# Performance work log

Measured on AMD Instinct MI355X. Metric: run time of the kernel, lower is better.

## Reference

```python
import jax, jax.numpy as jnp
import numpy as np

D, K = 128, 32
B, H, W = 16, 64, 64


def setup_inputs() -> dict:
    key = jax.random.key(0)
    k1, k2, k3 = jax.random.split(key, 3)
    x = jax.random.normal(k1, (B, D, H, W), dtype=jnp.float32)
    std1 = 1.0 / (K * D) ** 0.5
    codewords = jax.random.uniform(k2, (K, D), minval=-std1, maxval=std1, dtype=jnp.float32)
    scale = jax.random.uniform(k3, (K,), minval=-1.0, maxval=0.0, dtype=jnp.float32)
    return {"x": x, "codewords": codewords, "scale": scale}


def reference(x, codewords, scale):
    b = x.shape[0]
    # (B, D, H, W) -> (B, N, D)
    X = x.reshape(b, D, -1).transpose(0, 2, 1)
    # scaled L2: SL[b,n,k] = scale[k] * ||X[b,n] - C[k]||^2, expanded to avoid (B,N,K,D)
    x2 = jnp.sum(X * X, axis=-1)                      # (B, N)
    c2 = jnp.sum(codewords * codewords, axis=-1)      # (K,)
    xc = jnp.einsum('bnd,kd->bnk', X, codewords)      # (B, N, K)
    SL = scale[None, None, :] * (x2[:, :, None] - 2.0 * xc + c2[None, None, :])
    A = jax.nn.softmax(SL, axis=2)                    # (B, N, K)
    # E[b,k,d] = sum_n A[b,n,k] * (X[b,n,d] - C[k,d])
    E = jnp.einsum('bnk,bnd->bkd', A, X) - jnp.sum(A, axis=1)[:, :, None] * codewords[None, :, :]
    return E
```

## Files before the change

### kernel.cpp

```cpp
#include <hip/hip_runtime.h>
#include <hip/hip_bf16.h>


#define D_   128
#define K_   32
#define NPB  64
#define NTOT 4096

typedef __attribute__((ext_vector_type(8))) short bf16x8;
typedef __attribute__((ext_vector_type(4))) float f32x4;

__device__ __forceinline__ short f2b(float f) {
  unsigned u = __float_as_uint(f);
  unsigned r = (u + 0x7FFFu + ((u >> 16) & 1u)) >> 16;
  return (short)r;
}

__global__ __launch_bounds__(256, 4) void enc_kernel(
    const float* __restrict__ x,
    const float* __restrict__ cw,
    const float* __restrict__ scale,
    float* __restrict__ out)
{
  __shared__ __align__(16) float sX[D_ * NPB];
  __shared__ __align__(16) short sAb[K_ * NPB];
  __shared__ float sX2[NPB];
  __shared__ float sasum[K_];

  const int t  = threadIdx.x;
  const int w  = t >> 6;
  const int l  = t & 63;
  const int lr = l & 15;
  const int lg = l >> 4;
  const int b  = blockIdx.x >> 6;
  const int n0 = (blockIdx.x & 63) * NPB;

  if (t < K_) sasum[t] = 0.0f;

  const float* xb = x + (size_t)b * D_ * NTOT + n0;
  float4 xs[8];
  #pragma unroll
  for (int j = 0; j < 8; ++j) {
    int flat = j * 256 + t;
    int d = flat >> 4, n4 = flat & 15;
    xs[j] = *reinterpret_cast<const float4*>(xb + (size_t)d * NTOT + n4 * 4);
  }

  bf16x8 bC[2][4];
  float c2p0 = 0.f, c2p1 = 0.f;
  #pragma unroll
  for (int kt = 0; kt < 2; ++kt) {
    const float* crow = cw + (lr + 16 * kt) * D_ + lg * 8;
    #pragma unroll
    for (int s = 0; s < 4; ++s) {
      float4 v0 = *reinterpret_cast<const float4*>(crow + 32 * s);
      float4 v1 = *reinterpret_cast<const float4*>(crow + 32 * s + 4);
      float vv[8] = {v0.x, v0.y, v0.z, v0.w, v1.x, v1.y, v1.z, v1.w};
      bf16x8 f;
      float cs = 0.f;
      #pragma unroll
      for (int j = 0; j < 8; ++j) { f[j] = f2b(vv[j]); cs = fmaf(vv[j], vv[j], cs); }
      bC[kt][s] = f;
      if (kt == 0) c2p0 += cs; else c2p1 += cs;
    }
  }
  c2p0 += __shfl_xor(c2p0, 16); c2p0 += __shfl_xor(c2p0, 32);
  c2p1 += __shfl_xor(c2p1, 16); c2p1 += __shfl_xor(c2p1, 32);
  const float sc0 = scale[lr];
  const float sc1 = scale[lr + 16];

  float4* sX4 = reinterpret_cast<float4*>(sX);
  #pragma unroll
  for (int j = 0; j < 8; ++j) {
    int flat = j * 256 + t;
    int d = flat >> 4, n4 = flat & 15;
    sX4[d * 16 + (n4 ^ (d & 7))] = xs[j];
  }
  __syncthreads();

  const int m0 = w * 16;
  f32x4 p0 = {0.f, 0.f, 0.f, 0.f}, p1 = {0.f, 0.f, 0.f, 0.f};
  float x2p = 0.f;
  #pragma unroll
  for (int s = 0; s < 4; ++s) {
    int dbase = 32 * s + lg * 8;
    float av[8];
    #pragma unroll
    for (int j = 0; j < 8; ++j) {
      int d = dbase + j;
      av[j] = sX[d * 64 + ((m0 + lr) ^ ((d & 7) << 2))];
    }
    bf16x8 af;
    #pragma unroll
    for (int j = 0; j < 8; ++j) { af[j] = f2b(av[j]); x2p = fmaf(av[j], av[j], x2p); }
    p0 = __builtin_amdgcn_mfma_f32_16x16x32_bf16(af, bC[0][s], p0, 0, 0, 0);
    p1 = __builtin_amdgcn_mfma_f32_16x16x32_bf16(af, bC[1][s], p1, 0, 0, 0);
  }
  x2p += __shfl_xor(x2p, 16);
  x2p += __shfl_xor(x2p, 32);
  if (lg == 0) sX2[m0 + lr] = x2p;
  float x2r[4];
  #pragma unroll
  for (int r = 0; r < 4; ++r) x2r[r] = sX2[m0 + lg * 4 + r];

  float a0[4], a1[4], mr[4], sr[4];
  #pragma unroll
  for (int r = 0; r < 4; ++r) {
    float sl0 = sc0 * (x2r[r] - 2.f * p0[r] + c2p0);
    float sl1 = sc1 * (x2r[r] - 2.f * p1[r] + c2p1);
    a0[r] = sl0; a1[r] = sl1;
    mr[r] = fmaxf(sl0, sl1);
  }
  #pragma unroll
  for (int dlt = 1; dlt <= 8; dlt <<= 1)
    #pragma unroll
    for (int r = 0; r < 4; ++r) mr[r] = fmaxf(mr[r], __shfl_xor(mr[r], dlt));
  #pragma unroll
  for (int r = 0; r < 4; ++r) {
    a0[r] = __expf(a0[r] - mr[r]);
    a1[r] = __expf(a1[r] - mr[r]);
    sr[r] = a0[r] + a1[r];
  }
  #pragma unroll
  for (int dlt = 1; dlt <= 8; dlt <<= 1)
    #pragma unroll
    for (int r = 0; r < 4; ++r) sr[r] += __shfl_xor(sr[r], dlt);
  #pragma unroll
  for (int r = 0; r < 4; ++r) {
    float inv = 1.0f / sr[r];
    a0[r] *= inv; a1[r] *= inv;
  }

  float as0 = a0[0] + a0[1] + a0[2] + a0[3];
  float as1 = a1[0] + a1[1] + a1[2] + a1[3];
  as0 += __shfl_xor(as0, 16); as0 += __shfl_xor(as0, 32);
  as1 += __shfl_xor(as1, 16); as1 += __shfl_xor(as1, 32);
  if (lg == 0) {
    atomicAdd(&sasum[lr], as0);
    atomicAdd(&sasum[lr + 16], as1);
  }
  #pragma unroll
  for (int r = 0; r < 4; ++r) {
    int n = m0 + lg * 4 + r;
    int k0i = lr, k1i = lr + 16;
    sAb[k0i * 64 + (n ^ ((k0i & 7) << 3))] = f2b(a0[r]);
    sAb[k1i * 64 + (n ^ ((k1i & 7) << 3))] = f2b(a1[r]);
  }
  __syncthreads();

  bf16x8 aA[2][2];
  #pragma unroll
  for (int mt = 0; mt < 2; ++mt) {
    int k = mt * 16 + lr;
    #pragma unroll
    for (int s = 0; s < 2; ++s) {
      int nb = 32 * s + lg * 8;
      aA[mt][s] = *reinterpret_cast<const bf16x8*>(
          &sAb[k * 64 + (nb ^ ((k & 7) << 3))]);
    }
  }
  float asv[2][4];
  #pragma unroll
  for (int mt = 0; mt < 2; ++mt)
    #pragma unroll
    for (int r = 0; r < 4; ++r) asv[mt][r] = sasum[mt * 16 + lg * 4 + r];
  f32x4 acc[2][2];
  #pragma unroll
  for (int mt = 0; mt < 2; ++mt)
    #pragma unroll
    for (int dti = 0; dti < 2; ++dti) {
      int d = (2 * w + dti) * 16 + lr;
      #pragma unroll
      for (int r = 0; r < 4; ++r) {
        int k = mt * 16 + lg * 4 + r;
        acc[mt][dti][r] = -asv[mt][r] * cw[k * D_ + d];
      }
    }
  #pragma unroll
  for (int s = 0; s < 2; ++s) {
    #pragma unroll
    for (int dti = 0; dti < 2; ++dti) {
      int d = (2 * w + dti) * 16 + lr;
      int nb = 32 * s + lg * 8;
      int q0 = (nb >> 2) ^ (d & 7);
      int q1 = ((nb >> 2) + 1) ^ (d & 7);
      float4 v0 = sX4[d * 16 + q0];
      float4 v1 = sX4[d * 16 + q1];
      float vv[8] = {v0.x, v0.y, v0.z, v0.w, v1.x, v1.y, v1.z, v1.w};
      bf16x8 bf;
      #pragma unroll
      for (int j = 0; j < 8; ++j) bf[j] = f2b(vv[j]);
      acc[0][dti] = __builtin_amdgcn_mfma_f32_16x16x32_bf16(aA[0][s], bf, acc[0][dti], 0, 0, 0);
      acc[1][dti] = __builtin_amdgcn_mfma_f32_16x16x32_bf16(aA[1][s], bf, acc[1][dti], 0, 0, 0);
    }
  }
  float* op = out + (size_t)b * K_ * D_;
  #pragma unroll
  for (int mt = 0; mt < 2; ++mt)
    #pragma unroll
    for (int dti = 0; dti < 2; ++dti) {
      int d = (2 * w + dti) * 16 + lr;
      #pragma unroll
      for (int r = 0; r < 4; ++r) {
        int k = mt * 16 + lg * 4 + r;
        unsafeAtomicAdd(&op[k * D_ + d], acc[mt][dti][r]);
      }
    }
}

extern "C" void kernel_launch(void* const* d_in, const int* in_sizes, int n_in,
                              void* d_out, int out_size, void* d_ws, size_t ws_size,
                              hipStream_t stream) {
  const float* x  = (const float*)d_in[0];
  const float* cw = (const float*)d_in[1];
  const float* sc = (const float*)d_in[2];
  float* out = (float*)d_out;
  const int B = in_sizes[0] / (D_ * NTOT);
  hipMemsetAsync(d_out, 0, (size_t)out_size * sizeof(float), stream);
  enc_kernel<<<dim3(B * (NTOT / NPB)), dim3(256), 0, stream>>>(x, cw, sc, out);
}
```

Baseline: 92.22 us.

## Store x tile in shared memory as bf16 in both n-major and d-major layouts

```diff
diff --git a/kernel.cpp b/kernel.cpp
--- a/kernel.cpp
+++ b/kernel.cpp
@@ -9,11 +9,10 @@
 
 typedef __attribute__((ext_vector_type(8))) short bf16x8;
 typedef __attribute__((ext_vector_type(4))) float f32x4;
+typedef __attribute__((ext_vector_type(4))) short short4v;
 
 __device__ __forceinline__ short f2b(float f) {
-  unsigned u = __float_as_uint(f);
-  unsigned r = (u + 0x7FFFu + ((u >> 16) & 1u)) >> 16;
-  return (short)r;
+  return (short)__builtin_bit_cast(unsigned short, __float2bfloat16(f));
 }
 
 __global__ __launch_bounds__(256, 4) void enc_kernel(
@@ -22,9 +21,10 @@
     const float* __restrict__ scale,
     float* __restrict__ out)
 {
-  __shared__ __align__(16) float sX[D_ * NPB];
+  __shared__ __align__(16) short sNb[NPB * D_];
+  __shared__ __align__(16) short sDb[D_ * NPB];
   __shared__ __align__(16) short sAb[K_ * NPB];
-  __shared__ float sX2[NPB];
+  __shared__ __align__(16) float sX2w[NPB * 4];
   __shared__ float sasum[K_];
 
   const int t  = threadIdx.x;
@@ -37,13 +37,52 @@
 
   if (t < K_) sasum[t] = 0.0f;
 
+  const int n4s = t & 15;
+  const int d0  = (t >> 4) * 8;
   const float* xb = x + (size_t)b * D_ * NTOT + n0;
   float4 xs[8];
   #pragma unroll
+  for (int j = 0; j < 8; ++j)
+    xs[j] = *reinterpret_cast<const float4*>(xb + (size_t)(d0 + j) * NTOT + n4s * 4);
+
+  short xb16[8][4];
+  #pragma unroll
   for (int j = 0; j < 8; ++j) {
-    int flat = j * 256 + t;
-    int d = flat >> 4, n4 = flat & 15;
-    xs[j] = *reinterpret_cast<const float4*>(xb + (size_t)d * NTOT + n4 * 4);
+    xb16[j][0] = f2b(xs[j].x); xb16[j][1] = f2b(xs[j].y);
+    xb16[j][2] = f2b(xs[j].z); xb16[j][3] = f2b(xs[j].w);
+  }
+  float p2[4] = {0.f, 0.f, 0.f, 0.f};
+  #pragma unroll
+  for (int j = 0; j < 8; ++j) {
+    p2[0] = fmaf(xs[j].x, xs[j].x, p2[0]);
+    p2[1] = fmaf(xs[j].y, xs[j].y, p2[1]);
+    p2[2] = fmaf(xs[j].z, xs[j].z, p2[2]);
+    p2[3] = fmaf(xs[j].w, xs[j].w, p2[3]);
+  }
+  #pragma unroll
+  for (int i = 0; i < 4; ++i) {
+    p2[i] += __shfl_xor(p2[i], 16);
+    p2[i] += __shfl_xor(p2[i], 32);
+  }
+  if (lg == 0) {
+    #pragma unroll
+    for (int i = 0; i < 4; ++i) sX2w[(n4s * 4 + i) * 4 + w] = p2[i];
+  }
+  #pragma unroll
+  for (int i = 0; i < 4; ++i) {
+    int n = n4s * 4 + i;
+    bf16x8 pk;
+    #pragma unroll
+    for (int j = 0; j < 8; ++j) pk[j] = xb16[j][i];
+    int phys = ((d0 >> 3) ^ (n & 15)) & 15;
+    *reinterpret_cast<bf16x8*>(&sNb[n * D_ + phys * 8]) = pk;
+  }
+  #pragma unroll
+  for (int j = 0; j < 8; ++j) {
+    int d = d0 + j;
+    int phys = ((n4s >> 1) ^ (d & 7) ^ ((d >> 3) & 7)) & 7;
+    short4v pk4 = {xb16[j][0], xb16[j][1], xb16[j][2], xb16[j][3]};
+    *reinterpret_cast<short4v*>(&sDb[d * NPB + phys * 8 + (n4s & 1) * 4]) = pk4;
   }
 
   bf16x8 bC[2][4];
@@ -68,40 +107,25 @@
   c2p1 += __shfl_xor(c2p1, 16); c2p1 += __shfl_xor(c2p1, 32);
   const float sc0 = scale[lr];
   const float sc1 = scale[lr + 16];
-
-  float4* sX4 = reinterpret_cast<float4*>(sX);
-  #pragma unroll
-  for (int j = 0; j < 8; ++j) {
-    int flat = j * 256 + t;
-    int d = flat >> 4, n4 = flat & 15;
-    sX4[d * 16 + (n4 ^ (d & 7))] = xs[j];
-  }
   __syncthreads();
 
   const int m0 = w * 16;
+  const int nrow = m0 + lr;
   f32x4 p0 = {0.f, 0.f, 0.f, 0.f}, p1 = {0.f, 0.f, 0.f, 0.f};
-  float x2p = 0.f;
   #pragma unroll
   for (int s = 0; s < 4; ++s) {
-    int dbase = 32 * s + lg * 8;
-    float av[8];
-    #pragma unroll
-    for (int j = 0; j < 8; ++j) {
-      int d = dbase + j;
-      av[j] = sX[d * 64 + ((m0 + lr) ^ ((d & 7) << 2))];
-    }
-    bf16x8 af;
-    #pragma unroll
-    for (int j = 0; j < 8; ++j) { af[j] = f2b(av[j]); x2p = fmaf(av[j], av[j], x2p); }
+    int dblk = 4 * s + lg;
+    bf16x8 af = *reinterpret_cast<const bf16x8*>(
+        &sNb[nrow * D_ + ((dblk ^ lr) & 15) * 8]);
     p0 = __builtin_amdgcn_mfma_f32_16x16x32_bf16(af, bC[0][s], p0, 0, 0, 0);
     p1 = __builtin_amdgcn_mfma_f32_16x16x32_bf16(af, bC[1][s], p1, 0, 0, 0);
   }
-  x2p += __shfl_xor(x2p, 16);
-  x2p += __shfl_xor(x2p, 32);
-  if (lg == 0) sX2[m0 + lr] = x2p;
   float x2r[4];
   #pragma unroll
-  for (int r = 0; r < 4; ++r) x2r[r] = sX2[m0 + lg * 4 + r];
+  for (int r = 0; r < 4; ++r) {
+    float4 v = *reinterpret_cast<const float4*>(&sX2w[(m0 + lg * 4 + r) * 4]);
+    x2r[r] = (v.x + v.y) + (v.z + v.w);
+  }
 
   float a0[4], a1[4], mr[4], sr[4];
   #pragma unroll
@@ -142,9 +166,8 @@
   #pragma unroll
   for (int r = 0; r < 4; ++r) {
     int n = m0 + lg * 4 + r;
-    int k0i = lr, k1i = lr + 16;
-    sAb[k0i * 64 + (n ^ ((k0i & 7) << 3))] = f2b(a0[r]);
-    sAb[k1i * 64 + (n ^ ((k1i & 7) << 3))] = f2b(a1[r]);
+    sAb[lr * 64 + (n ^ ((lr & 7) << 3))] = f2b(a0[r]);
+    sAb[(lr + 16) * 64 + (n ^ (((lr + 16) & 7) << 3))] = f2b(a1[r]);
   }
   __syncthreads();
 
@@ -181,15 +204,8 @@
     #pragma unroll
     for (int dti = 0; dti < 2; ++dti) {
       int d = (2 * w + dti) * 16 + lr;
-      int nb = 32 * s + lg * 8;
-      int q0 = (nb >> 2) ^ (d & 7);
-      int q1 = ((nb >> 2) + 1) ^ (d & 7);
-      float4 v0 = sX4[d * 16 + q0];
-      float4 v1 = sX4[d * 16 + q1];
-      float vv[8] = {v0.x, v0.y, v0.z, v0.w, v1.x, v1.y, v1.z, v1.w};
-      bf16x8 bf;
-      #pragma unroll
-      for (int j = 0; j < 8; ++j) bf[j] = f2b(vv[j]);
+      int phys = (((4 * s + lg) ^ (d & 7) ^ ((d >> 3) & 7)) & 7);
+      bf16x8 bf = *reinterpret_cast<const bf16x8*>(&sDb[d * NPB + phys * 8]);
       acc[0][dti] = __builtin_amdgcn_mfma_f32_16x16x32_bf16(aA[0][s], bf, acc[0][dti], 0, 0, 0);
       acc[1][dti] = __builtin_amdgcn_mfma_f32_16x16x32_bf16(aA[1][s], bf, acc[1][dti], 0, 0, 0);
     }
```

Result: no change. 91.13 us (-1.2%).
